# Kernel tuning notes

Hardware: AMD Instinct MI355X
Metric: run time of the kernel (lower is better)

## Reference

```python
import jax, jax.numpy as jnp
import numpy as np
from jax import lax

N, CIN, COUT = 4, 3, 16
D = H = W = 64
K, S, PAD, OUT_PAD = 3, 2, 1, 1


def setup_inputs() -> dict:
    key = jax.random.key(0)
    k1, k2, k3, k4 = jax.random.split(key, 4)
    x = jax.random.normal(k1, (N, CIN, D, H, W), dtype=jnp.float32)
    # torch ConvTranspose3d weight layout: [Cin, Cout, kD, kH, kW]
    w = jax.random.normal(k2, (CIN, COUT, K, K, K), dtype=jnp.float32) * 0.1
    b = jax.random.normal(k3, (COUT,), dtype=jnp.float32) * 0.1
    subtract = jax.random.normal(k4, (COUT,), dtype=jnp.float32) * 0.1
    return {"x": x, "w": w, "b": b, "subtract": subtract}


def reference(x, w, b, subtract):
    # ConvTranspose3d(k=3, s=2, p=1, output_padding=1) as a dilated conv:
    # flip kernel spatially, swap in/out channel axes, lhs_dilation = stride,
    # padding low = k-1-p = 1, padding high = k-1-p+output_padding = 2.
    w_conv = jnp.flip(jnp.transpose(w, (1, 0, 2, 3, 4)), axis=(2, 3, 4))  # [Cout,Cin,k,k,k]
    y = lax.conv_general_dilated(
        x, w_conv,
        window_strides=(1, 1, 1),
        padding=[(1, 2), (1, 2), (1, 2)],
        lhs_dilation=(S, S, S),
        dimension_numbers=("NCDHW", "OIDHW", "NCDHW"),
    )  # [N, 16, 2D, 2H, 2W]
    y = y + b[None, :, None, None, None]
    # MaxPool3d(kernel=2, stride=2, pad=0)
    y = lax.reduce_window(
        y, -jnp.inf, lax.max,
        window_dimensions=(1, 1, 2, 2, 2),
        window_strides=(1, 1, 2, 2, 2),
        padding="VALID",
    )  # [N, 16, D, H, W]
    s = jax.nn.softmax(y, axis=1)                       # channel softmax
    z = s - subtract[None, :, None, None, None]          # per-channel subtract
    sw = z * jax.nn.sigmoid(z)                           # swish
    return jnp.max(sw, axis=1)                           # max over channels -> [N, D, H, W]
```

## Files before the change

kernel.cpp:

```cpp
#include <hip/hip_runtime.h>
#include <math.h>

#define CIN   3
#define COUT  16
#define DHW   64

__global__ __launch_bounds__(256, 2) void fused_convt_pool_softmax_swish_max(
    const float* __restrict__ x,
    const float* __restrict__ w,
    const float* __restrict__ bias,
    const float* __restrict__ sub,
    float* __restrict__ out)
{
    const int tp = threadIdx.x;
    const int h  = blockIdx.x * blockDim.y + threadIdx.y;
    const int d  = blockIdx.y;
    const int n  = blockIdx.z;
    const int w0 = tp * 2;

    float xr[CIN][2][2][3];
    const size_t nbase = (size_t)n * CIN * DHW * DHW * DHW;
    const bool w2ok = (w0 + 2 < DHW);
    const int  off2 = w2ok ? 2 : 0;
#pragma unroll
    for (int c = 0; c < CIN; ++c) {
#pragma unroll
        for (int dd = 0; dd < 2; ++dd) {
#pragma unroll
            for (int hh = 0; hh < 2; ++hh) {
                const int id = d + dd;
                const int ih = h + hh;
                float v0 = 0.0f, v1 = 0.0f, v2 = 0.0f;
                if (id < DHW && ih < DHW) {
                    const float* row = x + nbase + (((size_t)c * DHW + id) * DHW + ih) * DHW + w0;
                    const float2 a = *(const float2*)row;
                    v0 = a.x;
                    v1 = a.y;
                    const float t = row[off2];
                    v2 = w2ok ? t : 0.0f;
                }
                xr[c][dd][hh][0] = v0;
                xr[c][dd][hh][1] = v1;
                xr[c][dd][hh][2] = v2;
            }
        }
    }

    float pooled[2][COUT];
#pragma unroll
    for (int co = 0; co < COUT; ++co) {
        float acc[2][2][2][2];
#pragma unroll
        for (int v = 0; v < 2; ++v)
#pragma unroll
            for (int i = 0; i < 8; ++i)
                (&acc[v][0][0][0])[i] = 0.0f;
#pragma unroll
        for (int c = 0; c < CIN; ++c) {
            const float* wp = w + ((size_t)(c * COUT + co)) * 27;
#pragma unroll
            for (int kd = 0; kd < 3; ++kd) {
                const int pd = (kd == 1) ? 0 : 1;
                const int dd = (kd == 0) ? 1 : 0;
#pragma unroll
                for (int kh = 0; kh < 3; ++kh) {
                    const int ph = (kh == 1) ? 0 : 1;
                    const int hh = (kh == 0) ? 1 : 0;
#pragma unroll
                    for (int kw = 0; kw < 3; ++kw) {
                        const int pw = (kw == 1) ? 0 : 1;
                        const int ww = (kw == 0) ? 1 : 0;
                        const float wt = wp[kd * 9 + kh * 3 + kw];
#pragma unroll
                        for (int v = 0; v < 2; ++v)
                            acc[v][pd][ph][pw] =
                                fmaf(wt, xr[c][dd][hh][v + ww], acc[v][pd][ph][pw]);
                    }
                }
            }
        }
        const float bco = bias[co];
#pragma unroll
        for (int v = 0; v < 2; ++v) {
            const float* a = &acc[v][0][0][0];
            const float m0 = fmaxf(fmaxf(a[0], a[1]), a[2]);
            const float m1 = fmaxf(fmaxf(a[3], a[4]), a[5]);
            const float m2 = fmaxf(fmaxf(a[6], a[7]), m0);
            pooled[v][co] = fmaxf(m1, m2) + bco;
        }
    }

    float res[2];
#pragma unroll
    for (int v = 0; v < 2; ++v) {
        float m = pooled[v][0];
#pragma unroll
        for (int co = 1; co < COUT; ++co) m = fmaxf(m, pooled[v][co]);
        float e[COUT];
        float s = 0.0f;
#pragma unroll
        for (int co = 0; co < COUT; ++co) {
            e[co] = __expf(pooled[v][co] - m);
            s += e[co];
        }
        const float inv = __builtin_amdgcn_rcpf(s);
        float zmax = -3.402823466e+38f;
#pragma unroll
        for (int co = 0; co < COUT; ++co)
            zmax = fmaxf(zmax, fmaf(e[co], inv, -sub[co]));
        res[v] = zmax * __builtin_amdgcn_rcpf(1.0f + __expf(-zmax));
    }

    float* op = out + (((size_t)n * DHW + d) * DHW + h) * DHW + w0;
    *(float2*)op = make_float2(res[0], res[1]);
}

extern "C" void kernel_launch(void* const* d_in, const int* in_sizes, int n_in,
                              void* d_out, int out_size, void* d_ws, size_t ws_size,
                              hipStream_t stream) {
    const float* x   = (const float*)d_in[0];
    const float* w   = (const float*)d_in[1];
    const float* b   = (const float*)d_in[2];
    const float* sub = (const float*)d_in[3];
    float* out = (float*)d_out;

    dim3 block(32, 8, 1);
    dim3 grid(DHW / 8, DHW, 4);
    fused_convt_pool_softmax_swish_max<<<grid, block, 0, stream>>>(x, w, b, sub, out);
}
```

Before: 108.8 us.

## Stage weights in LDS in packed layout and use v_pk_fma_f32 for depth pairs

Copies the transposed-conv weights into shared memory, rearranged so the kd=1/kd=2 taps form adjacent pairs. Inputs are packed into depth pairs, so one packed FMA (inline asm v_pk_fma_f32 with the x operand splatted) updates both depth parities, plus one scalar FMA for the kd=0 tap. This removes many scalar global weight loads and roughly halves the FMA instruction count. It adds per-block LDS staging with a barrier, inline asm, and raises launch bounds to 3 blocks per CU.

```diff
diff --git a/kernel.cpp b/kernel.cpp
--- a/kernel.cpp
+++ b/kernel.cpp
@@ -4,44 +4,64 @@
 #define CIN   3
 #define COUT  16
 #define DHW   64
+#define WPAD  28
 
-__global__ __launch_bounds__(256, 2) void fused_convt_pool_softmax_swish_max(
+typedef float v2f __attribute__((ext_vector_type(2)));
+
+#define PK_FMA_XSPLAT(acc, w2, x2) \
+    asm("v_pk_fma_f32 %0, %1, %2, %0 op_sel_hi:[1,0,1]" : "+v"(acc) : "v"(w2), "v"(x2))
+
+__global__ __launch_bounds__(256, 3) void fused_convt_pool_softmax_swish_max(
     const float* __restrict__ x,
     const float* __restrict__ w,
     const float* __restrict__ bias,
     const float* __restrict__ sub,
     float* __restrict__ out)
 {
-    const int tp = threadIdx.x;
+    __shared__ float wsm[CIN * COUT * WPAD];
+
+    const int tid = threadIdx.y * 32 + threadIdx.x;
+    for (int i = tid; i < CIN * COUT * 27; i += 256) {
+        const int g  = i / 27, r = i - g * 27;
+        const int kd = r / 9,  j = r - kd * 9;
+        const int slot = (kd == 0) ? (18 + j) : (2 * j + (kd - 1));
+        wsm[g * WPAD + slot] = w[i];
+    }
+    __syncthreads();
+
+    const int tx = threadIdx.x;
     const int h  = blockIdx.x * blockDim.y + threadIdx.y;
     const int d  = blockIdx.y;
     const int n  = blockIdx.z;
-    const int w0 = tp * 2;
+    const int w0 = tx * 2;
 
-    float xr[CIN][2][2][3];
+    v2f P[CIN][2][3];
     const size_t nbase = (size_t)n * CIN * DHW * DHW * DHW;
     const bool w2ok = (w0 + 2 < DHW);
     const int  off2 = w2ok ? 2 : 0;
 #pragma unroll
     for (int c = 0; c < CIN; ++c) {
 #pragma unroll
-        for (int dd = 0; dd < 2; ++dd) {
+        for (int hh = 0; hh < 2; ++hh) {
+            float vd[2][3];
 #pragma unroll
-            for (int hh = 0; hh < 2; ++hh) {
+            for (int dd = 0; dd < 2; ++dd) {
                 const int id = d + dd;
                 const int ih = h + hh;
-                float v0 = 0.0f, v1 = 0.0f, v2 = 0.0f;
+                float v0 = 0.f, v1 = 0.f, v2 = 0.f;
                 if (id < DHW && ih < DHW) {
                     const float* row = x + nbase + (((size_t)c * DHW + id) * DHW + ih) * DHW + w0;
                     const float2 a = *(const float2*)row;
-                    v0 = a.x;
-                    v1 = a.y;
+                    v0 = a.x; v1 = a.y;
                     const float t = row[off2];
                     v2 = w2ok ? t : 0.0f;
                 }
-                xr[c][dd][hh][0] = v0;
-                xr[c][dd][hh][1] = v1;
-                xr[c][dd][hh][2] = v2;
+                vd[dd][0] = v0; vd[dd][1] = v1; vd[dd][2] = v2;
+            }
+#pragma unroll
+            for (int jw = 0; jw < 3; ++jw) {
+                v2f p; p.x = vd[0][jw]; p.y = vd[1][jw];
+                P[c][hh][jw] = p;
             }
         }
     }
@@ -49,32 +69,33 @@
     float pooled[2][COUT];
 #pragma unroll
     for (int co = 0; co < COUT; ++co) {
-        float acc[2][2][2][2];
+        v2f acc[2][2][2];
 #pragma unroll
-        for (int v = 0; v < 2; ++v)
-#pragma unroll
-            for (int i = 0; i < 8; ++i)
-                (&acc[v][0][0][0])[i] = 0.0f;
+        for (int i = 0; i < 8; ++i) { v2f z; z.x = 0.f; z.y = 0.f; (&acc[0][0][0])[i] = z; }
 #pragma unroll
         for (int c = 0; c < CIN; ++c) {
-            const float* wp = w + ((size_t)(c * COUT + co)) * 27;
+            const float4* wq4 = (const float4*)&wsm[(c * COUT + co) * WPAD];
+            float4 qw[7];
 #pragma unroll
-            for (int kd = 0; kd < 3; ++kd) {
-                const int pd = (kd == 1) ? 0 : 1;
-                const int dd = (kd == 0) ? 1 : 0;
+            for (int t = 0; t < 7; ++t) qw[t] = wq4[t];
+            const v2f*   wp2 = (const v2f*)&qw[0];
+            const float* wf  = (const float*)&qw[0];
 #pragma unroll
-                for (int kh = 0; kh < 3; ++kh) {
-                    const int ph = (kh == 1) ? 0 : 1;
-                    const int hh = (kh == 0) ? 1 : 0;
+            for (int kh = 0; kh < 3; ++kh) {
+                const int ph = (kh == 1) ? 0 : 1;
+                const int hh = (kh == 0) ? 1 : 0;
 #pragma unroll
-                    for (int kw = 0; kw < 3; ++kw) {
-                        const int pw = (kw == 1) ? 0 : 1;
-                        const int ww = (kw == 0) ? 1 : 0;
-                        const float wt = wp[kd * 9 + kh * 3 + kw];
+                for (int kw = 0; kw < 3; ++kw) {
+                    const int pw = (kw == 1) ? 0 : 1;
+                    const int ww = (kw == 0) ? 1 : 0;
+                    const int j  = kh * 3 + kw;
+                    const v2f   wpair = wp2[j];
+                    const float wsgl  = wf[18 + j];
 #pragma unroll
-                        for (int v = 0; v < 2; ++v)
-                            acc[v][pd][ph][pw] =
-                                fmaf(wt, xr[c][dd][hh][v + ww], acc[v][pd][ph][pw]);
+                    for (int v = 0; v < 2; ++v) {
+                        const v2f xp = P[c][hh][v + ww];
+                        PK_FMA_XSPLAT(acc[v][ph][pw], wpair, xp);
+                        acc[v][ph][pw].y = fmaf(wsgl, xp.y, acc[v][ph][pw].y);
                     }
                 }
             }
@@ -82,11 +103,10 @@
         const float bco = bias[co];
 #pragma unroll
         for (int v = 0; v < 2; ++v) {
-            const float* a = &acc[v][0][0][0];
-            const float m0 = fmaxf(fmaxf(a[0], a[1]), a[2]);
-            const float m1 = fmaxf(fmaxf(a[3], a[4]), a[5]);
-            const float m2 = fmaxf(fmaxf(a[6], a[7]), m0);
-            pooled[v][co] = fmaxf(m1, m2) + bco;
+            v2f m01 = __builtin_elementwise_max(acc[v][0][0], acc[v][0][1]);
+            v2f m23 = __builtin_elementwise_max(acc[v][1][0], acc[v][1][1]);
+            v2f mm  = __builtin_elementwise_max(m01, m23);
+            pooled[v][co] = fmaxf(mm.x, mm.y) + bco;
         }
     }
 
```

After: 105.4 us. 1.03x faster.

## Use packed FP32 FMA over channel pairs with LDS-staged weights and 4 outputs/thread

Applied to the files above, without the earlier changes.

Each thread now computes four output columns instead of two, and the block is halved to 128 threads. Weights are staged in LDS, interleaved by output-channel pairs, so v_pk_fma_f32 can process two channels per instruction through inline asm with op_sel broadcasting the input value. The pooled results go through LDS, presumably to ease register pressure before the softmax. This targets FMA issue throughput and scalar weight loads, at the cost of more register pressure, LDS traffic, a block-wide barrier and fewer threads per block.

```diff
diff --git a/kernel.cpp b/kernel.cpp
--- a/kernel.cpp
+++ b/kernel.cpp
@@ -4,24 +4,46 @@
 #define CIN   3
 #define COUT  16
 #define DHW   64
+#define NCP   8
+#define GP    56
 
-__global__ __launch_bounds__(256, 2) void fused_convt_pool_softmax_swish_max(
+typedef float v2f __attribute__((ext_vector_type(2)));
+
+#define PK_FMA_XLO(acc, w2, x2) \
+    asm("v_pk_fma_f32 %0, %1, %2, %0 op_sel_hi:[1,0,1]" : "+v"(acc) : "v"(w2), "v"(x2))
+#define PK_FMA_XHI(acc, w2, x2) \
+    asm("v_pk_fma_f32 %0, %1, %2, %0 op_sel:[0,1,0] op_sel_hi:[1,1,1]" : "+v"(acc) : "v"(w2), "v"(x2))
+
+__global__ __launch_bounds__(128, 2) void fused_convt_pool_softmax_swish_max(
     const float* __restrict__ x,
     const float* __restrict__ w,
     const float* __restrict__ bias,
     const float* __restrict__ sub,
     float* __restrict__ out)
 {
-    const int tp = threadIdx.x;
-    const int h  = blockIdx.x * blockDim.y + threadIdx.y;
+    __shared__ float  wsm[CIN * NCP * GP];
+    __shared__ float4 plds[NCP][2][128];
+
+    const int tid = threadIdx.y * 16 + threadIdx.x;
+    for (int i = tid; i < CIN * COUT * 27; i += 128) {
+        const int c   = i / (COUT * 27);
+        const int rem = i - c * COUT * 27;
+        const int co  = rem / 27;
+        const int t   = rem - co * 27;
+        wsm[(c * NCP + (co >> 1)) * GP + 2 * t + (co & 1)] = w[i];
+    }
+    __syncthreads();
+
+    const int tx = threadIdx.x;
+    const int h  = blockIdx.x * 8 + threadIdx.y;
     const int d  = blockIdx.y;
     const int n  = blockIdx.z;
-    const int w0 = tp * 2;
+    const int w0 = tx * 4;
 
-    float xr[CIN][2][2][3];
+    v2f X[CIN][2][2][3];
     const size_t nbase = (size_t)n * CIN * DHW * DHW * DHW;
-    const bool w2ok = (w0 + 2 < DHW);
-    const int  off2 = w2ok ? 2 : 0;
+    const bool w4ok = (w0 + 4 < DHW);
+    const int  off4 = w4ok ? 4 : 0;
 #pragma unroll
     for (int c = 0; c < CIN; ++c) {
 #pragma unroll
@@ -30,34 +52,36 @@
             for (int hh = 0; hh < 2; ++hh) {
                 const int id = d + dd;
                 const int ih = h + hh;
-                float v0 = 0.0f, v1 = 0.0f, v2 = 0.0f;
+                float4 q = make_float4(0.f, 0.f, 0.f, 0.f);
+                float x4 = 0.0f;
                 if (id < DHW && ih < DHW) {
                     const float* row = x + nbase + (((size_t)c * DHW + id) * DHW + ih) * DHW + w0;
-                    const float2 a = *(const float2*)row;
-                    v0 = a.x;
-                    v1 = a.y;
-                    const float t = row[off2];
-                    v2 = w2ok ? t : 0.0f;
+                    q = *(const float4*)row;
+                    const float t = row[off4];
+                    x4 = w4ok ? t : 0.0f;
                 }
-                xr[c][dd][hh][0] = v0;
-                xr[c][dd][hh][1] = v1;
-                xr[c][dd][hh][2] = v2;
+                v2f p0; p0.x = q.x; p0.y = q.y;
+                v2f p1; p1.x = q.z; p1.y = q.w;
+                v2f p2; p2.x = x4;  p2.y = 0.0f;
+                X[c][dd][hh][0] = p0;
+                X[c][dd][hh][1] = p1;
+                X[c][dd][hh][2] = p2;
             }
         }
     }
 
-    float pooled[2][COUT];
 #pragma unroll
-    for (int co = 0; co < COUT; ++co) {
-        float acc[2][2][2][2];
+    for (int cp = 0; cp < NCP; ++cp) {
+        v2f acc[4][2][2][2];
 #pragma unroll
-        for (int v = 0; v < 2; ++v)
-#pragma unroll
-            for (int i = 0; i < 8; ++i)
-                (&acc[v][0][0][0])[i] = 0.0f;
+        for (int i = 0; i < 32; ++i) { v2f z; z.x = 0.f; z.y = 0.f; (&acc[0][0][0][0])[i] = z; }
 #pragma unroll
         for (int c = 0; c < CIN; ++c) {
-            const float* wp = w + ((size_t)(c * COUT + co)) * 27;
+            const float4* wq4 = (const float4*)&wsm[(c * NCP + cp) * GP];
+            float4 qw[14];
+#pragma unroll
+            for (int t = 0; t < 14; ++t) qw[t] = wq4[t];
+            const v2f* wp = (const v2f*)&qw[0];
 #pragma unroll
             for (int kd = 0; kd < 3; ++kd) {
                 const int pd = (kd == 1) ? 0 : 1;
@@ -70,29 +94,53 @@
                     for (int kw = 0; kw < 3; ++kw) {
                         const int pw = (kw == 1) ? 0 : 1;
                         const int ww = (kw == 0) ? 1 : 0;
-                        const float wt = wp[kd * 9 + kh * 3 + kw];
+                        const int t  = kd * 9 + kh * 3 + kw;
 #pragma unroll
-                        for (int v = 0; v < 2; ++v)
-                            acc[v][pd][ph][pw] =
-                                fmaf(wt, xr[c][dd][hh][v + ww], acc[v][pd][ph][pw]);
+                        for (int v = 0; v < 4; ++v) {
+                            const int e  = v + ww;
+                            const int pe = e >> 1;
+                            if ((e & 1) == 0) {
+                                PK_FMA_XLO(acc[v][pd][ph][pw], wp[t], X[c][dd][hh][pe]);
+                            } else {
+                                PK_FMA_XHI(acc[v][pd][ph][pw], wp[t], X[c][dd][hh][pe]);
+                            }
+                        }
                     }
                 }
             }
         }
-        const float bco = bias[co];
+        v2f bp; bp.x = bias[2 * cp]; bp.y = bias[2 * cp + 1];
+        v2f mm[4];
 #pragma unroll
-        for (int v = 0; v < 2; ++v) {
-            const float* a = &acc[v][0][0][0];
-            const float m0 = fmaxf(fmaxf(a[0], a[1]), a[2]);
-            const float m1 = fmaxf(fmaxf(a[3], a[4]), a[5]);
-            const float m2 = fmaxf(fmaxf(a[6], a[7]), m0);
-            pooled[v][co] = fmaxf(m1, m2) + bco;
+        for (int v = 0; v < 4; ++v) {
+            const v2f* a = &acc[v][0][0][0];
+            v2f m0 = __builtin_elementwise_max(__builtin_elementwise_max(a[0], a[1]),
+                                               __builtin_elementwise_max(a[2], a[3]));
+            v2f m1 = __builtin_elementwise_max(__builtin_elementwise_max(a[4], a[5]),
+                                               __builtin_elementwise_max(a[6], a[7]));
+            mm[v] = __builtin_elementwise_max(m0, m1) + bp;
         }
+        float4 p01; p01.x = mm[0].x; p01.y = mm[0].y; p01.z = mm[1].x; p01.w = mm[1].y;
+        float4 p23; p23.x = mm[2].x; p23.y = mm[2].y; p23.z = mm[3].x; p23.w = mm[3].y;
+        plds[cp][0][tid] = p01;
+        plds[cp][1][tid] = p23;
     }
 
-    float res[2];
+    float pooled[4][COUT];
 #pragma unroll
-    for (int v = 0; v < 2; ++v) {
+    for (int cp = 0; cp < NCP; ++cp) {
+        const float4 qa = plds[cp][0][tid];
+        const float4 qb = plds[cp][1][tid];
+        pooled[0][2 * cp] = qa.x; pooled[0][2 * cp + 1] = qa.y;
+        pooled[1][2 * cp] = qa.z; pooled[1][2 * cp + 1] = qa.w;
+        pooled[2][2 * cp] = qb.x; pooled[2][2 * cp + 1] = qb.y;
+        pooled[3][2 * cp] = qb.z; pooled[3][2 * cp + 1] = qb.w;
+    }
+
+    float4 resq;
+    float* resf = (float*)&resq;
+#pragma unroll
+    for (int v = 0; v < 4; ++v) {
         float m = pooled[v][0];
 #pragma unroll
         for (int co = 1; co < COUT; ++co) m = fmaxf(m, pooled[v][co]);
@@ -108,11 +156,11 @@
 #pragma unroll
         for (int co = 0; co < COUT; ++co)
             zmax = fmaxf(zmax, fmaf(e[co], inv, -sub[co]));
-        res[v] = zmax * __builtin_amdgcn_rcpf(1.0f + __expf(-zmax));
+        resf[v] = zmax * __builtin_amdgcn_rcpf(1.0f + __expf(-zmax));
     }
 
     float* op = out + (((size_t)n * DHW + d) * DHW + h) * DHW + w0;
-    *(float2*)op = make_float2(res[0], res[1]);
+    *(float4*)op = resq;
 }
 
 extern "C" void kernel_launch(void* const* d_in, const int* in_sizes, int n_in,
@@ -124,7 +172,7 @@
     const float* sub = (const float*)d_in[3];
     float* out = (float*)d_out;
 
-    dim3 block(32, 8, 1);
+    dim3 block(16, 8, 1);
     dim3 grid(DHW / 8, DHW, 4);
     fused_convt_pool_softmax_swish_max<<<grid, block, 0, stream>>>(x, w, b, sub, out);
 }
```

New measurement: 112.9 us. 3.8% more time.
